# Optimization experiments

Measured on AMD Instinct MI355X. Metric: run time of the kernel, lower is better.

## Reference

```python
import jax, jax.numpy as jnp
import numpy as np

B, S, D = 4, 2048, 1024
H = 16
HD = D // H
DFF = 4096
MAX_REL = 32
EPS = 1e-5


def _rms_norm(x, w):
    rms = jnp.sqrt(jnp.mean(x * x, axis=-1, keepdims=True) + EPS)
    return x / rms * w


def setup_inputs() -> dict:
    key = jax.random.key(0)
    ks = jax.random.split(key, 16)
    sc = 0.02
    d = {
        "x": jax.random.normal(ks[0], (B, S, D), dtype=jnp.float32),
        "g1": jnp.ones((D,), dtype=jnp.float32),
        "g2": jnp.ones((D,), dtype=jnp.float32),
        "wq": jax.random.normal(ks[1], (D, D), dtype=jnp.float32) * sc,
        "bq": jnp.zeros((D,), dtype=jnp.float32),
        "wk": jax.random.normal(ks[2], (D, D), dtype=jnp.float32) * sc,
        "bk": jnp.zeros((D,), dtype=jnp.float32),
        "wv": jax.random.normal(ks[3], (D, D), dtype=jnp.float32) * sc,
        "bv": jnp.zeros((D,), dtype=jnp.float32),
        "wo": jax.random.normal(ks[4], (D, D), dtype=jnp.float32) * sc,
        "bo": jnp.zeros((D,), dtype=jnp.float32),
        "rel_pos": jax.random.normal(ks[5], (H, 2 * MAX_REL + 1), dtype=jnp.float32),
        "w1": jax.random.normal(ks[6], (D, DFF), dtype=jnp.float32) * sc,
        "b1": jnp.zeros((DFF,), dtype=jnp.float32),
        "w2": jax.random.normal(ks[7], (DFF, D), dtype=jnp.float32) * sc,
        "b2": jnp.zeros((D,), dtype=jnp.float32),
    }
    return d


def reference(x, g1, g2, wq, bq, wk, bk, wv, bv, wo, bo, rel_pos, w1, b1, w2, b2):
    b, s, d = x.shape
    # --- multi-head attention with relative-position bias ---
    q = (x @ wq + bq).reshape(b, s, H, HD).transpose(0, 2, 1, 3)  # [B,H,S,HD]
    k = (x @ wk + bk).reshape(b, s, H, HD).transpose(0, 2, 1, 3)
    v = (x @ wv + bv).reshape(b, s, H, HD).transpose(0, 2, 1, 3)
    scores = jnp.einsum("bhqd,bhkd->bhqk", q, k) / jnp.sqrt(jnp.float32(HD))
    # relative position bias: gather from (H, 2*MAX_REL+1) table
    pos = jnp.arange(s)
    rel = pos[None, :] - pos[:, None]                # [S,S]
    idx = jnp.clip(rel, -MAX_REL, MAX_REL) + MAX_REL  # [S,S]
    bias = rel_pos[:, idx]                            # [H,S,S]
    scores = scores + bias[None]
    attn = jax.nn.softmax(scores, axis=-1)
    out = jnp.einsum("bhqk,bhkd->bhqd", attn, v)
    out = out.transpose(0, 2, 1, 3).reshape(b, s, d)
    attn_out = out @ wo + bo
    # residual + RMSNorm
    x = _rms_norm(attn_out + x, g1)
    # --- feed-forward (exact GELU) ---
    h = jax.nn.gelu(x @ w1 + b1, approximate=False)
    ff = h @ w2 + b2
    x = _rms_norm(ff + x, g2)
    return x
```

## Files before the change

kernel.cpp:

```cpp
#include <hip/hip_runtime.h>

#define B_ 4
#define S_ 2048
#define D_ 1024
#define H_ 16
#define HD_ 64
#define DFF_ 4096
#define MR_ 32
#define M_ (B_*S_)

typedef unsigned short u16;
typedef __attribute__((ext_vector_type(8))) short bf16x8;
typedef __attribute__((ext_vector_type(4))) float f32x4;

#define MFMA16 __builtin_amdgcn_mfma_f32_16x16x32_bf16
#define A_CONST 0.18033688011112f
#define LOG2E_ 1.44269504088896f

__device__ __forceinline__ u16 f2b(float f) {
  unsigned u = __builtin_bit_cast(unsigned, f);
  u = u + 0x7FFFu + ((u >> 16) & 1u);
  return (u16)(u >> 16);
}
__device__ __forceinline__ float b2f(u16 h) {
  unsigned u = ((unsigned)h) << 16;
  return __builtin_bit_cast(float, u);
}
__device__ __forceinline__ float exp2_fast(float x) {
  float r;
  asm("v_exp_f32 %0, %1" : "=v"(r) : "v"(x));
  return r;
}
__device__ __forceinline__ unsigned cvtpk(float lo, float hi) {
  unsigned r;
  asm("v_cvt_pk_bf16_f32 %0, %1, %2" : "=v"(r) : "v"(lo), "v"(hi));
  return r;
}
__device__ __forceinline__ float max3f(float a, float b, float c) {
  float r;
  asm("v_max3_f32 %0, %1, %2, %3" : "=v"(r) : "v"(a), "v"(b), "v"(c));
  return r;
}
__device__ __forceinline__ int med3i(int a, int b, int c) {
  int r;
  asm("v_med3_i32 %0, %1, %2, %3" : "=v"(r) : "v"(a), "v"(b), "v"(c));
  return r;
}
__device__ __forceinline__ void gl_lds16(const void* g, void* l) {
  __builtin_amdgcn_global_load_lds(
      (const __attribute__((address_space(1))) void*)g,
      (__attribute__((address_space(3))) void*)l, 16, 0, 0);
}

#define SWZ(r) ((((((r)>>3)&1)<<2) ^ ((r)&7)) << 4)
#define SWZ64(r) ((((r)>>1)&3) << 4)

__global__ __launch_bounds__(256) void cvt_kernel(const float* __restrict__ in,
                                                  u16* __restrict__ out, int n4) {
  int i = blockIdx.x * 256 + threadIdx.x;
  if (i < n4) {
    float4 v = ((const float4*)in)[i];
    ushort4 o;
    o.x = f2b(v.x); o.y = f2b(v.y); o.z = f2b(v.z); o.w = f2b(v.w);
    ((ushort4*)out)[i] = o;
  }
}

__global__ __launch_bounds__(256) void wtrans_kernel(const float* __restrict__ in,
                                                     u16* __restrict__ out, int R, int C) {
  __shared__ float t[32][33];
  int c0 = blockIdx.x * 32, r0 = blockIdx.y * 32;
  int x = threadIdx.x, y = threadIdx.y;
#pragma unroll
  for (int i = 0; i < 4; ++i)
    t[y + i*8][x] = in[(long)(r0 + y + i*8) * C + c0 + x];
  __syncthreads();
#pragma unroll
  for (int i = 0; i < 4; ++i)
    out[(long)(c0 + y + i*8) * R + r0 + x] = f2b(t[x][y + i*8]);
}

__global__ __launch_bounds__(256) void vtrans_kernel(const u16* __restrict__ v,
                                                     u16* __restrict__ vT) {
  __shared__ u16 t[32][33];
  int bh = blockIdx.y; int b = bh >> 4, h = bh & 15;
  int s0 = (blockIdx.x >> 1) * 32;
  int d0 = (blockIdx.x & 1) * 32;
  int x = threadIdx.x, y = threadIdx.y;
#pragma unroll
  for (int i = 0; i < 4; ++i)
    t[y + i*8][x] = v[((long)(b*S_ + s0 + y + i*8)) * D_ + h*64 + d0 + x];
  __syncthreads();
#pragma unroll
  for (int i = 0; i < 4; ++i)
    vT[((long)((b*H_ + h)*HD_ + d0 + y + i*8)) * S_ + s0 + x] = t[x][y + i*8];
}

template<int EPI, int WN>
__global__ __launch_bounds__(512, 2) void gemm9(
    const u16* __restrict__ A, const u16* __restrict__ BT,
    const float* __restrict__ bias0, const float* __restrict__ bias1,
    const float* __restrict__ bias2,
    u16* __restrict__ C0, u16* __restrict__ C1, u16* __restrict__ C2,
    int Ndim, int Kdim)
{
  constexpr int BN = WN * 64;
  constexpr int WM = 8 / WN;
  constexpr int MROWS = 256 / WM;
  constexpr int MF = MROWS / 16;
  __shared__ char lds[4][32768];
  const int tid = threadIdx.x;
  const int w = tid >> 6, lane = tid & 63;
  const int lr = lane & 15, lg = lane >> 4;
  const int wm = w / WN, wn = w % WN;

  const int nbx = Ndim / BN;
  const int cpx = gridDim.x >> 3;
  const int bid = blockIdx.x;
  const int swzb = (bid & 7) * cpx + (bid >> 3);
  const long blockM = (long)(swzb / nbx) * 256;
  const long blockN = (long)(swzb % nbx) * BN;

  const int srow = tid >> 2;
  const int scol = ((tid & 3) * 16) ^ SWZ64(srow);
  const u16* Ag  = A + (blockM + srow) * (long)Kdim + (scol >> 1);
  const u16* Ag2 = Ag + (long)128 * Kdim;
  const u16* Bg  = BT + (blockN + srow) * (long)Kdim + (scol >> 1);
  const u16* Bg2 = Bg + (long)128 * Kdim;
  char* const ldsAw = &lds[0][0] + w * 1024;
  char* const ldsBw = &lds[0][0] + 16384 + w * 1024;

#define STAGE_A(t) { char* d_=ldsAw+((t)&3)*32768; const long ko_=(long)(t)*32; \
    gl_lds16(Ag  + ko_, d_); gl_lds16(Ag2 + ko_, d_ + 8192); }
#define STAGE_B(t) { char* d_=ldsBw+((t)&3)*32768; const long ko_=(long)(t)*32; \
    gl_lds16(Bg  + ko_, d_); if constexpr (WN==4) gl_lds16(Bg2 + ko_, d_ + 8192); }

  const int rsw = (lg * 16) ^ SWZ64(lr);
  int offA[MF], offB[4];
#pragma unroll
  for (int mf = 0; mf < MF; ++mf) offA[mf] = (wm*MROWS + mf*16 + lr) * 64 + rsw;
#pragma unroll
  for (int nf = 0; nf < 4; ++nf)  offB[nf] = 16384 + (wn*64 + nf*16 + lr) * 64 + rsw;

  f32x4 acc[MF][4] = {};
  const int NS = Kdim >> 5;

  STAGE_A(0); STAGE_B(0); STAGE_A(1); STAGE_B(1);
  if (WN == 4) asm volatile("s_waitcnt vmcnt(4)" ::: "memory");
  else         asm volatile("s_waitcnt vmcnt(3)" ::: "memory");
  __builtin_amdgcn_s_barrier();

  for (int t = 0; t < NS; ++t) {
    const char* sl = &lds[t & 3][0];
    bf16x8 af[MF], bfr[4];
    if constexpr (WN == 4) {
#pragma unroll
      for (int mf = 0; mf < MF; ++mf) af[mf] = *(const bf16x8*)(sl + offA[mf]);
      bfr[0] = *(const bf16x8*)(sl + offB[0]);
      bfr[1] = *(const bf16x8*)(sl + offB[1]);
      if (t + 2 < NS) STAGE_A(t + 2);
      __builtin_amdgcn_s_barrier();
      __builtin_amdgcn_s_setprio(1);
#pragma unroll
      for (int mf = 0; mf < MF; ++mf) acc[mf][0] = MFMA16(bfr[0], af[mf], acc[mf][0], 0, 0, 0);
#pragma unroll
      for (int mf = 0; mf < MF; ++mf) acc[mf][1] = MFMA16(bfr[1], af[mf], acc[mf][1], 0, 0, 0);
      __builtin_amdgcn_s_setprio(0);
      __builtin_amdgcn_s_barrier();
      bfr[2] = *(const bf16x8*)(sl + offB[2]);
      bfr[3] = *(const bf16x8*)(sl + offB[3]);
      if (t + 2 < NS) {
        STAGE_B(t + 2);
        asm volatile("s_waitcnt vmcnt(4)" ::: "memory");
      } else if (t == NS - 2) {
        asm volatile("s_waitcnt vmcnt(0)" ::: "memory");
      }
      __builtin_amdgcn_s_barrier();
      __builtin_amdgcn_s_setprio(1);
#pragma unroll
      for (int mf = 0; mf < MF; ++mf) acc[mf][2] = MFMA16(bfr[2], af[mf], acc[mf][2], 0, 0, 0);
#pragma unroll
      for (int mf = 0; mf < MF; ++mf) acc[mf][3] = MFMA16(bfr[3], af[mf], acc[mf][3], 0, 0, 0);
      __builtin_amdgcn_s_setprio(0);
      __builtin_amdgcn_s_barrier();
    } else {
#pragma unroll
      for (int mf = 0; mf < MF; ++mf) af[mf] = *(const bf16x8*)(sl + offA[mf]);
#pragma unroll
      for (int nf = 0; nf < 4; ++nf)  bfr[nf] = *(const bf16x8*)(sl + offB[nf]);
      if (t + 2 < NS) {
        STAGE_A(t + 2); STAGE_B(t + 2);
        asm volatile("s_waitcnt vmcnt(3)" ::: "memory");
      } else if (t == NS - 2) {
        asm volatile("s_waitcnt vmcnt(0)" ::: "memory");
      }
      __builtin_amdgcn_s_barrier();
      __builtin_amdgcn_s_setprio(1);
#pragma unroll
      for (int mf = 0; mf < MF; ++mf)
#pragma unroll
        for (int nf = 0; nf < 4; ++nf)
          acc[mf][nf] = MFMA16(bfr[nf], af[mf], acc[mf][nf], 0, 0, 0);
      __builtin_amdgcn_s_setprio(0);
      __builtin_amdgcn_s_barrier();
    }
  }

  const float* bsel = bias0;
  u16* osel = C0;
  long nstride = Ndim;
  long ncol0 = blockN;
  if (EPI == 3) {
    int mat = (int)(blockN >> 10);
    bsel = mat == 0 ? bias0 : (mat == 1 ? bias1 : bias2);
    osel = mat == 0 ? C0 : (mat == 1 ? C1 : C2);
    nstride = 1024;
    ncol0 = blockN & 1023;
  }
  const long row0 = blockM + wm*MROWS;
#pragma unroll
  for (int mf = 0; mf < MF; ++mf) {
    long row = row0 + mf*16 + lr;
#pragma unroll
    for (int nf = 0; nf < 4; ++nf) {
      long col = ncol0 + wn*64 + nf*16 + lg*4;
      float4 bv = *(const float4*)&bsel[col];
      float v0 = acc[mf][nf][0] + bv.x;
      float v1 = acc[mf][nf][1] + bv.y;
      float v2 = acc[mf][nf][2] + bv.z;
      float v3 = acc[mf][nf][3] + bv.w;
      if (EPI == 2) {
        v0 = 0.5f*v0*(1.0f + erff(v0*0.70710678118654752f));
        v1 = 0.5f*v1*(1.0f + erff(v1*0.70710678118654752f));
        v2 = 0.5f*v2*(1.0f + erff(v2*0.70710678118654752f));
        v3 = 0.5f*v3*(1.0f + erff(v3*0.70710678118654752f));
      }
      ushort4 st;
      st.x = f2b(v0); st.y = f2b(v1); st.z = f2b(v2); st.w = f2b(v3);
      *(ushort4*)&osel[row * nstride + col] = st;
    }
  }
#undef STAGE_A
#undef STAGE_B
}

__device__ __forceinline__ float max16v(const f32x4* s) {
  float a = max3f(s[0][0], s[0][1], s[0][2]);
  float b = max3f(s[0][3], s[1][0], s[1][1]);
  float c = max3f(s[1][2], s[1][3], s[2][0]);
  float d = max3f(s[2][1], s[2][2], s[2][3]);
  float e = max3f(s[3][0], s[3][1], s[3][2]);
  float f = max3f(a, b, s[3][3]);
  float g = max3f(c, d, e);
  return fmaxf(f, g);
}
__device__ __forceinline__ float max16s(const float* v) {
  float a = max3f(v[0], v[1], v[2]);
  float b = max3f(v[3], v[4], v[5]);
  float c = max3f(v[6], v[7], v[8]);
  float d = max3f(v[9], v[10], v[11]);
  float e = max3f(v[12], v[13], v[14]);
  float f = max3f(a, b, v[15]);
  float g = max3f(c, d, e);
  return fmaxf(f, g);
}

__device__ __forceinline__ void sm_finish(float* p, float& l_r, bf16x8* pfo) {
  float ls = ((p[0]+p[1])+(p[2]+p[3])) + ((p[4]+p[5])+(p[6]+p[7]))
           + ((p[8]+p[9])+(p[10]+p[11])) + ((p[12]+p[13])+(p[14]+p[15]));
  ls += __shfl_xor(ls, 16);
  ls += __shfl_xor(ls, 32);
  l_r += ls;
#pragma unroll
  for (int ks = 0; ks < 2; ++ks) {
    uint4 uu;
    uu.x = cvtpk(p[ks*4+0], p[ks*4+1]);
    uu.y = cvtpk(p[ks*4+2], p[ks*4+3]);
    uu.z = cvtpk(p[(ks+2)*4+0], p[(ks+2)*4+1]);
    uu.w = cvtpk(p[(ks+2)*4+2], p[(ks+2)*4+3]);
    pfo[ks] = __builtin_bit_cast(bf16x8, uu);
  }
}

__device__ __forceinline__ void softmax_uni(const f32x4* s, float bu,
    float& m_r, float& l_r, f32x4* acc, bf16x8* pfo)
{
  float mx = fmaf(max16v(s), A_CONST, bu);
  mx = fmaxf(mx, __shfl_xor(mx, 16));
  mx = fmaxf(mx, __shfl_xor(mx, 32));
  if (!__all(mx <= m_r + 8.0f)) {
    float mn = fmaxf(m_r, mx);
    float sc = exp2_fast(m_r - mn);
    m_r = mn;
    l_r *= sc;
#pragma unroll
    for (int ni = 0; ni < 4; ++ni) acc[ni] *= sc;
  }
  float cc = bu - m_r;
  float p[16];
#pragma unroll
  for (int ni = 0; ni < 4; ++ni)
#pragma unroll
    for (int j = 0; j < 4; ++j)
      p[ni*4+j] = exp2_fast(fmaf(s[ni][j], A_CONST, cc));
  sm_finish(p, l_r, pfo);
}

__device__ __forceinline__ void softmax_slow(const f32x4* s, const float* relb,
    int rbase, float& m_r, float& l_r, f32x4* acc, bf16x8* pfo)
{
  float sv[16];
#pragma unroll
  for (int ni = 0; ni < 4; ++ni) {
    const int koff = (ni&1)*32 + (ni>>1)*4;
#pragma unroll
    for (int j = 0; j < 4; ++j) {
      int idx = med3i(rbase + koff + j + MR_, 0, 2*MR_);
      sv[ni*4+j] = fmaf(s[ni][j], A_CONST, relb[idx]);
    }
  }
  float mx = max16s(sv);
  mx = fmaxf(mx, __shfl_xor(mx, 16));
  mx = fmaxf(mx, __shfl_xor(mx, 32));
  if (!__all(mx <= m_r + 8.0f)) {
    float mn = fmaxf(m_r, mx);
    float sc = exp2_fast(m_r - mn);
    m_r = mn;
    l_r *= sc;
#pragma unroll
    for (int ni = 0; ni < 4; ++ni) acc[ni] *= sc;
  }
  float p[16];
#pragma unroll
  for (int i = 0; i < 16; ++i) p[i] = exp2_fast(sv[i] - m_r);
  sm_finish(p, l_r, pfo);
}

__global__ __launch_bounds__(256, 4) void attn3_kernel(
    const u16* __restrict__ q, const u16* __restrict__ k,
    const u16* __restrict__ vT, const float* __restrict__ rel_pos,
    u16* __restrict__ ao)
{
  __shared__ u16 KB[2][4096];
  __shared__ u16 VB[2][4096];
  __shared__ float relb[2*MR_ + 1];

  const int tid = threadIdx.x;
  const int w = tid >> 6, lane = tid & 63;
  const int lr = lane & 15, lg = lane >> 4;
  const int qt = blockIdx.x, bh = blockIdx.y;
  const int b = bh >> 4, h = bh & 15;
  const int q0 = qt * 128;
  const int qq = q0 + w*32;

  if (tid < 2*MR_ + 1) relb[tid] = rel_pos[h * (2*MR_ + 1) + tid] * LOG2E_;

  const int srow0 = w*8 + (lane >> 3);
  const int srow1 = 32 + srow0;
  const int scb   = (lane & 7) * 16;
  const int col0  = scb ^ SWZ(srow0);
  const int col1  = scb ^ SWZ(srow1);

  const long qkbase = ((long)(b*S_)) * D_ + h*64;
  const long vbase  = ((long)((b*H_ + h) * HD_)) * S_;

  {
    const u16* qg = q + qkbase + (long)q0 * D_;
#pragma unroll
    for (int c = 0; c < 4; ++c) {
      int row = c*32 + srow0;
      int colc = scb ^ SWZ(row);
      gl_lds16(qg + (long)row*D_ + (colc >> 1), &KB[0][0] + (c*32 + w*8)*64);
    }
  }
  __syncthreads();
  bf16x8 qf[4];
#pragma unroll
  for (int qi = 0; qi < 2; ++qi)
#pragma unroll
    for (int ks = 0; ks < 2; ++ks) {
      int row = w*32 + qi*16 + lr;
      qf[qi*2+ks] = *(const bf16x8*)((const char*)&KB[0][0] + row*128 + ((ks*64 + lg*16) ^ SWZ(row)));
    }
  const float bHI = relb[2*MR_];
  const float bLO = relb[0];
  __syncthreads();

  int offK0[4], offV0[4];
#pragma unroll
  for (int ni = 0; ni < 4; ++ni) {
    int kr = (ni&1)*32 + (lr>>2)*8 + (ni>>1)*4 + (lr&3);
    int vr = ni*16 + lr;
    offK0[ni] = kr*128 + ((lg*16) ^ SWZ(kr));
    offV0[ni] = vr*128 + ((lg*16) ^ SWZ(vr));
  }

  const u16* kp0 = k  + qkbase + (long)srow0*D_ + (col0 >> 1);
  const u16* kp1 = k  + qkbase + (long)srow1*D_ + (col1 >> 1);
  const u16* vp0 = vT + vbase  + (long)srow0*S_ + (col0 >> 1);
  const u16* vp1 = vT + vbase  + (long)srow1*S_ + (col1 >> 1);
  u16* kb_w0 = &KB[0][(w*8)*64];
  u16* kb_w1 = &KB[0][(32 + w*8)*64];
  u16* vb_w0 = &VB[0][(w*8)*64];
  u16* vb_w1 = &VB[0][(32 + w*8)*64];

  float m_r[2] = {-1e30f, -1e30f};
  float l_r[2] = {0.f, 0.f};
  f32x4 acco[2][4] = {};

  gl_lds16(kp0, kb_w0);
  gl_lds16(kp1, kb_w1);
  gl_lds16(vp0, vb_w0);
  gl_lds16(vp1, vb_w1);

  const long kstep = (long)64 * D_;
  const int NT = S_ / 64;
  for (int t = 0; t < NT; ++t) {
    const int cur = t & 1;
    __syncthreads();
    if (t + 1 < NT) {
      int bufo = (cur ^ 1) * 4096;
      gl_lds16(kp0 + (long)(t+1)*kstep, kb_w0 + bufo);
      gl_lds16(kp1 + (long)(t+1)*kstep, kb_w1 + bufo);
      gl_lds16(vp0 + (t+1)*64, vb_w0 + bufo);
      gl_lds16(vp1 + (t+1)*64, vb_w1 + bufo);
    }
    const char* Kb = (const char*)&KB[cur][0];
    const char* Vb = (const char*)&VB[cur][0];
    const int k0 = t * 64;

    f32x4 s0[4] = {}, s1[4] = {};
#pragma unroll
    for (int ks = 0; ks < 2; ++ks)
#pragma unroll
      for (int ni = 0; ni < 4; ++ni) {
        bf16x8 kf = *(const bf16x8*)(Kb + (offK0[ni] ^ (ks*64)));
        s0[ni] = MFMA16(kf, qf[ks],   s0[ni], 0, 0, 0);
        s1[ni] = MFMA16(kf, qf[2+ks], s1[ni], 0, 0, 0);
      }

    bf16x8 pf0[2], pf1[2];
    bool hi_u = (k0 - (qq + 31)) >= MR_;
    bool lo_u = (qq - (k0 + 63)) >= MR_;
    if (hi_u || lo_u) {
      float bu = hi_u ? bHI : bLO;
      softmax_uni(s0, bu, m_r[0], l_r[0], acco[0], pf0);
      softmax_uni(s1, bu, m_r[1], l_r[1], acco[1], pf1);
    } else {
      int rb0 = k0 + lg*8 - (qq + lr);
      softmax_slow(s0, relb, rb0,      m_r[0], l_r[0], acco[0], pf0);
      softmax_slow(s1, relb, rb0 - 16, m_r[1], l_r[1], acco[1], pf1);
    }

#pragma unroll
    for (int ks = 0; ks < 2; ++ks)
#pragma unroll
      for (int ni = 0; ni < 4; ++ni) {
        bf16x8 vf = *(const bf16x8*)(Vb + (offV0[ni] ^ (ks*64)));
        acco[0][ni] = MFMA16(vf, pf0[ks], acco[0][ni], 0, 0, 0);
        acco[1][ni] = MFMA16(vf, pf1[ks], acco[1][ni], 0, 0, 0);
      }
  }

#pragma unroll
  for (int qi = 0; qi < 2; ++qi) {
    float inv = 1.0f / l_r[qi];
    long orow = ((long)(b*S_ + qq + qi*16 + lr)) * D_ + h*64;
#pragma unroll
    for (int ni = 0; ni < 4; ++ni) {
      ushort4 ov;
      ov.x = f2b(acco[qi][ni][0] * inv);
      ov.y = f2b(acco[qi][ni][1] * inv);
      ov.z = f2b(acco[qi][ni][2] * inv);
      ov.w = f2b(acco[qi][ni][3] * inv);
      *(ushort4*)(ao + orow + ni*16 + lg*4) = ov;
    }
  }
}

template<int ABF, int BBF>
__global__ __launch_bounds__(256) void rmsnorm_kernel(
    const void* __restrict__ a, const void* __restrict__ b,
    const float* __restrict__ g, float* __restrict__ outf,
    u16* __restrict__ outb)
{
  long row = blockIdx.x;
  int tid = threadIdx.x;
  float ya[4], yb[4], y[4];
  if (ABF) {
    ushort4 av = ((const ushort4*)a)[row*256 + tid];
    ya[0] = b2f(av.x); ya[1] = b2f(av.y); ya[2] = b2f(av.z); ya[3] = b2f(av.w);
  } else {
    float4 av = ((const float4*)a)[row*256 + tid];
    ya[0] = av.x; ya[1] = av.y; ya[2] = av.z; ya[3] = av.w;
  }
  if (BBF) {
    ushort4 bv = ((const ushort4*)b)[row*256 + tid];
    yb[0] = b2f(bv.x); yb[1] = b2f(bv.y); yb[2] = b2f(bv.z); yb[3] = b2f(bv.w);
  } else {
    float4 bv = ((const float4*)b)[row*256 + tid];
    yb[0] = bv.x; yb[1] = bv.y; yb[2] = bv.z; yb[3] = bv.w;
  }
  float ss = 0.f;
#pragma unroll
  for (int i = 0; i < 4; ++i) { y[i] = ya[i] + yb[i]; ss += y[i]*y[i]; }
#pragma unroll
  for (int m = 1; m < 64; m <<= 1) ss += __shfl_xor(ss, m);
  __shared__ float red[4];
  int w = tid >> 6, lane = tid & 63;
  if (lane == 0) red[w] = ss;
  __syncthreads();
  ss = red[0] + red[1] + red[2] + red[3];
  float rinv = rsqrtf(ss * (1.0f / D_) + 1e-5f);
  float4 gv = ((const float4*)g)[tid];
  float o[4] = { y[0]*rinv*gv.x, y[1]*rinv*gv.y, y[2]*rinv*gv.z, y[3]*rinv*gv.w };
  if (outf) {
    float4 of = { o[0], o[1], o[2], o[3] };
    ((float4*)outf)[row*256 + tid] = of;
  }
  if (outb) {
    ushort4 ob;
    ob.x = f2b(o[0]); ob.y = f2b(o[1]); ob.z = f2b(o[2]); ob.w = f2b(o[3]);
    ((ushort4*)outb)[row*256 + tid] = ob;
  }
}

extern "C" void kernel_launch(void* const* d_in, const int* in_sizes, int n_in,
                              void* d_out, int out_size, void* d_ws, size_t ws_size,
                              hipStream_t stream) {
  const float* x   = (const float*)d_in[0];
  const float* g1  = (const float*)d_in[1];
  const float* g2  = (const float*)d_in[2];
  const float* wq  = (const float*)d_in[3];
  const float* bq  = (const float*)d_in[4];
  const float* wk  = (const float*)d_in[5];
  const float* bk  = (const float*)d_in[6];
  const float* wv  = (const float*)d_in[7];
  const float* bv  = (const float*)d_in[8];
  const float* wo  = (const float*)d_in[9];
  const float* bo  = (const float*)d_in[10];
  const float* rel = (const float*)d_in[11];
  const float* w1  = (const float*)d_in[12];
  const float* b1  = (const float*)d_in[13];
  const float* w2  = (const float*)d_in[14];
  const float* b2  = (const float*)d_in[15];
  float* out = (float*)d_out;

  char* ws = (char*)d_ws;
  const size_t MB = 1024ull * 1024ull;
  u16* xb   = (u16*)(ws + 0);
  u16* wqT  = (u16*)(ws + 16*MB);
  u16* wkT  = (u16*)(ws + 18*MB);
  u16* wvT  = (u16*)(ws + 20*MB);
  u16* woT  = (u16*)(ws + 22*MB);
  u16* w1T  = (u16*)(ws + 24*MB);
  u16* w2T  = (u16*)(ws + 32*MB);
  u16* qb   = (u16*)(ws + 40*MB);
  u16* kb   = (u16*)(ws + 56*MB);
  u16* vb   = (u16*)(ws + 72*MB);
  u16* vTb  = (u16*)(ws + 88*MB);
  u16* aob  = (u16*)(ws + 104*MB);
  u16* prjb = (u16*)(ws + 120*MB);
  u16* x1b  = (u16*)(ws + 136*MB);
  u16* hb   = (u16*)(ws + 40*MB);
  u16* ffb  = (u16*)(ws + 120*MB);
  (void)ws_size; (void)in_sizes; (void)n_in; (void)out_size;

  dim3 tb(32, 8);

  cvt_kernel<<<M_*D_/4/256, 256, 0, stream>>>(x, xb, M_*D_/4);
  wtrans_kernel<<<dim3(D_/32,   D_/32),   tb, 0, stream>>>(wq, wqT, D_,   D_);
  wtrans_kernel<<<dim3(D_/32,   D_/32),   tb, 0, stream>>>(wk, wkT, D_,   D_);
  wtrans_kernel<<<dim3(D_/32,   D_/32),   tb, 0, stream>>>(wv, wvT, D_,   D_);
  wtrans_kernel<<<dim3(D_/32,   D_/32),   tb, 0, stream>>>(wo, woT, D_,   D_);
  wtrans_kernel<<<dim3(DFF_/32, D_/32),   tb, 0, stream>>>(w1, w1T, D_,   DFF_);
  wtrans_kernel<<<dim3(D_/32,   DFF_/32), tb, 0, stream>>>(w2, w2T, DFF_, D_);

  gemm9<3,4><<<(3072/256)*(M_/256), 512, 0, stream>>>(
      xb, wqT, bq, bk, bv, qb, kb, vb, 3072, D_);

  vtrans_kernel<<<dim3((S_/32)*(HD_/32), B_*H_), tb, 0, stream>>>(vb, vTb);

  attn3_kernel<<<dim3(S_/128, B_*H_), 256, 0, stream>>>(qb, kb, vTb, rel, aob);

  gemm9<0,2><<<(D_/128)*(M_/256), 512, 0, stream>>>(
      aob, woT, bo, nullptr, nullptr, prjb, nullptr, nullptr, D_, D_);

  rmsnorm_kernel<1,0><<<M_, 256, 0, stream>>>(prjb, x, g1, nullptr, x1b);

  gemm9<2,4><<<(DFF_/256)*(M_/256), 512, 0, stream>>>(
      x1b, w1T, b1, nullptr, nullptr, hb, nullptr, nullptr, DFF_, D_);

  gemm9<0,2><<<(D_/128)*(M_/256), 512, 0, stream>>>(
      hb, w2T, b2, nullptr, nullptr, ffb, nullptr, nullptr, D_, DFF_);

  rmsnorm_kernel<1,1><<<M_, 256, 0, stream>>>(ffb, x1b, g2, out, nullptr);
}
```

Before: 450.5 us.

## Compute softmax row sums via MFMA, shuffle rel-bias, stage GEMM epilogue through LDS

Attention now gets the softmax denominator from an extra MFMA against a ones vector, which removes the per-tile scalar sums and cross-lane shuffles. The relative-position bias table lives in registers and is read with lane shuffles instead of an LDS table. Occupancy is raised to 5 waves via launch bounds. The GEMM epilogue now writes results into swizzled LDS and then stores coalesced 16-byte rows, at the cost of an extra barrier and LDS traffic.

```diff
diff --git a/kernel.cpp b/kernel.cpp
--- a/kernel.cpp
+++ b/kernel.cpp
@@ -217,14 +217,15 @@
     nstride = 1024;
     ncol0 = blockN & 1023;
   }
-  const long row0 = blockM + wm*MROWS;
+  constexpr int RB = BN * 2;
+  char* const et = &lds[0][0];
 #pragma unroll
   for (int mf = 0; mf < MF; ++mf) {
-    long row = row0 + mf*16 + lr;
+    const int row = wm*MROWS + mf*16 + lr;
 #pragma unroll
     for (int nf = 0; nf < 4; ++nf) {
-      long col = ncol0 + wn*64 + nf*16 + lg*4;
-      float4 bv = *(const float4*)&bsel[col];
+      const int colu = wn*64 + nf*16 + lg*4;
+      float4 bv = *(const float4*)&bsel[ncol0 + colu];
       float v0 = acc[mf][nf][0] + bv.x;
       float v1 = acc[mf][nf][1] + bv.y;
       float v2 = acc[mf][nf][2] + bv.z;
@@ -237,8 +238,19 @@
       }
       ushort4 st;
       st.x = f2b(v0); st.y = f2b(v1); st.z = f2b(v2); st.w = f2b(v3);
-      *(ushort4*)&osel[row * nstride + col] = st;
-    }
+      *(ushort4*)(et + row*RB + ((colu*2) ^ ((row & 7) << 4))) = st;
+    }
+  }
+  __syncthreads();
+  constexpr int CHR  = RB / 16;
+  constexpr int ITER = 256 * CHR / 512;
+#pragma unroll
+  for (int i = 0; i < ITER; ++i) {
+    const int idx = i*512 + tid;
+    const int row = idx / CHR;
+    const int cb  = (idx % CHR) * 16;
+    uint4 val = *(const uint4*)(et + row*RB + (cb ^ ((row & 7) << 4)));
+    *(uint4*)&osel[(blockM + row) * nstride + ncol0 + (cb >> 1)] = val;
   }
 #undef STAGE_A
 #undef STAGE_B
@@ -265,12 +277,7 @@
   return fmaxf(f, g);
 }
 
-__device__ __forceinline__ void sm_finish(float* p, float& l_r, bf16x8* pfo) {
-  float ls = ((p[0]+p[1])+(p[2]+p[3])) + ((p[4]+p[5])+(p[6]+p[7]))
-           + ((p[8]+p[9])+(p[10]+p[11])) + ((p[12]+p[13])+(p[14]+p[15]));
-  ls += __shfl_xor(ls, 16);
-  ls += __shfl_xor(ls, 32);
-  l_r += ls;
+__device__ __forceinline__ void packp(const float* p, bf16x8* pfo) {
 #pragma unroll
   for (int ks = 0; ks < 2; ++ks) {
     uint4 uu;
@@ -283,7 +290,7 @@
 }
 
 __device__ __forceinline__ void softmax_uni(const f32x4* s, float bu,
-    float& m_r, float& l_r, f32x4* acc, bf16x8* pfo)
+    float& m_r, f32x4* acc, bf16x8* pfo)
 {
   float mx = fmaf(max16v(s), A_CONST, bu);
   mx = fmaxf(mx, __shfl_xor(mx, 16));
@@ -292,9 +299,8 @@
     float mn = fmaxf(m_r, mx);
     float sc = exp2_fast(m_r - mn);
     m_r = mn;
-    l_r *= sc;
-#pragma unroll
-    for (int ni = 0; ni < 4; ++ni) acc[ni] *= sc;
+#pragma unroll
+    for (int ni = 0; ni < 5; ++ni) acc[ni] *= sc;
   }
   float cc = bu - m_r;
   float p[16];
@@ -303,11 +309,11 @@
 #pragma unroll
     for (int j = 0; j < 4; ++j)
       p[ni*4+j] = exp2_fast(fmaf(s[ni][j], A_CONST, cc));
-  sm_finish(p, l_r, pfo);
-}
-
-__device__ __forceinline__ void softmax_slow(const f32x4* s, const float* relb,
-    int rbase, float& m_r, float& l_r, f32x4* acc, bf16x8* pfo)
+  packp(p, pfo);
+}
+
+__device__ __forceinline__ void softmax_slow(const f32x4* s, float rp, float bHI,
+    int rbase, float& m_r, f32x4* acc, bf16x8* pfo)
 {
   float sv[16];
 #pragma unroll
@@ -316,7 +322,9 @@
 #pragma unroll
     for (int j = 0; j < 4; ++j) {
       int idx = med3i(rbase + koff + j + MR_, 0, 2*MR_);
-      sv[ni*4+j] = fmaf(s[ni][j], A_CONST, relb[idx]);
+      float bb = __shfl(rp, idx);
+      bb = (idx >= 64) ? bHI : bb;
+      sv[ni*4+j] = fmaf(s[ni][j], A_CONST, bb);
     }
   }
   float mx = max16s(sv);
@@ -326,24 +334,22 @@
     float mn = fmaxf(m_r, mx);
     float sc = exp2_fast(m_r - mn);
     m_r = mn;
-    l_r *= sc;
-#pragma unroll
-    for (int ni = 0; ni < 4; ++ni) acc[ni] *= sc;
+#pragma unroll
+    for (int ni = 0; ni < 5; ++ni) acc[ni] *= sc;
   }
   float p[16];
 #pragma unroll
   for (int i = 0; i < 16; ++i) p[i] = exp2_fast(sv[i] - m_r);
-  sm_finish(p, l_r, pfo);
-}
-
-__global__ __launch_bounds__(256, 4) void attn3_kernel(
+  packp(p, pfo);
+}
+
+__global__ __launch_bounds__(256, 5) void attn4_kernel(
     const u16* __restrict__ q, const u16* __restrict__ k,
     const u16* __restrict__ vT, const float* __restrict__ rel_pos,
     u16* __restrict__ ao)
 {
   __shared__ u16 KB[2][4096];
   __shared__ u16 VB[2][4096];
-  __shared__ float relb[2*MR_ + 1];
 
   const int tid = threadIdx.x;
   const int w = tid >> 6, lane = tid & 63;
@@ -353,7 +359,9 @@
   const int q0 = qt * 128;
   const int qq = q0 + w*32;
 
-  if (tid < 2*MR_ + 1) relb[tid] = rel_pos[h * (2*MR_ + 1) + tid] * LOG2E_;
+  const float rp  = rel_pos[h*(2*MR_+1) + lane] * LOG2E_;
+  const float bHI = rel_pos[h*(2*MR_+1) + 2*MR_] * LOG2E_;
+  const float bLO = __shfl(rp, 0);
 
   const int srow0 = w*8 + (lane >> 3);
   const int srow1 = 32 + srow0;
@@ -382,8 +390,6 @@
       int row = w*32 + qi*16 + lr;
       qf[qi*2+ks] = *(const bf16x8*)((const char*)&KB[0][0] + row*128 + ((ks*64 + lg*16) ^ SWZ(row)));
     }
-  const float bHI = relb[2*MR_];
-  const float bLO = relb[0];
   __syncthreads();
 
   int offK0[4], offV0[4];
@@ -404,9 +410,12 @@
   u16* vb_w0 = &VB[0][(w*8)*64];
   u16* vb_w1 = &VB[0][(32 + w*8)*64];
 
+  bf16x8 onesf;
+#pragma unroll
+  for (int i = 0; i < 8; ++i) onesf[i] = (short)0x3F80;
+
   float m_r[2] = {-1e30f, -1e30f};
-  float l_r[2] = {0.f, 0.f};
-  f32x4 acco[2][4] = {};
+  f32x4 acco[2][5] = {};
 
   gl_lds16(kp0, kb_w0);
   gl_lds16(kp1, kb_w1);
@@ -444,27 +453,30 @@
     bool lo_u = (qq - (k0 + 63)) >= MR_;
     if (hi_u || lo_u) {
       float bu = hi_u ? bHI : bLO;
-      softmax_uni(s0, bu, m_r[0], l_r[0], acco[0], pf0);
-      softmax_uni(s1, bu, m_r[1], l_r[1], acco[1], pf1);
+      softmax_uni(s0, bu, m_r[0], acco[0], pf0);
+      softmax_uni(s1, bu, m_r[1], acco[1], pf1);
     } else {
       int rb0 = k0 + lg*8 - (qq + lr);
-      softmax_slow(s0, relb, rb0,      m_r[0], l_r[0], acco[0], pf0);
-      softmax_slow(s1, relb, rb0 - 16, m_r[1], l_r[1], acco[1], pf1);
-    }
-
-#pragma unroll
-    for (int ks = 0; ks < 2; ++ks)
+      softmax_slow(s0, rp, bHI, rb0,      m_r[0], acco[0], pf0);
+      softmax_slow(s1, rp, bHI, rb0 - 16, m_r[1], acco[1], pf1);
+    }
+
+#pragma unroll
+    for (int ks = 0; ks < 2; ++ks) {
 #pragma unroll
       for (int ni = 0; ni < 4; ++ni) {
         bf16x8 vf = *(const bf16x8*)(Vb + (offV0[ni] ^ (ks*64)));
         acco[0][ni] = MFMA16(vf, pf0[ks], acco[0][ni], 0, 0, 0);
         acco[1][ni] = MFMA16(vf, pf1[ks], acco[1][ni], 0, 0, 0);
       }
+      acco[0][4] = MFMA16(onesf, pf0[ks], acco[0][4], 0, 0, 0);
+      acco[1][4] = MFMA16(onesf, pf1[ks], acco[1][4], 0, 0, 0);
+    }
   }
 
 #pragma unroll
   for (int qi = 0; qi < 2; ++qi) {
-    float inv = 1.0f / l_r[qi];
+    float inv = 1.0f / acco[qi][4][0];
     long orow = ((long)(b*S_ + qq + qi*16 + lr)) * D_ + h*64;
 #pragma unroll
     for (int ni = 0; ni < 4; ++ni) {
@@ -581,7 +593,7 @@
 
   vtrans_kernel<<<dim3((S_/32)*(HD_/32), B_*H_), tb, 0, stream>>>(vb, vTb);
 
-  attn3_kernel<<<dim3(S_/128, B_*H_), 256, 0, stream>>>(qb, kb, vTb, rel, aob);
+  attn4_kernel<<<dim3(S_/128, B_*H_), 256, 0, stream>>>(qb, kb, vTb, rel, aob);
 
   gemm9<0,2><<<(D_/128)*(M_/256), 512, 0, stream>>>(
       aob, woT, bo, nullptr, nullptr, prjb, nullptr, nullptr, D_, D_);
```

After: 740.5 us. +64.4%, slower.
